# Kernel tuning notes

Measured on AMD Instinct MI355X. Metric: run time of the kernel, lower is better.

Reference implementation:

```python
import jax, jax.numpy as jnp
from jax import lax
import numpy as np


def _conv1d(x, w, b):
    # x: (N, C, L), w: (O, I, K), stride 2, padding 1 -> matches nn.Conv1d(k=4, s=2, p=1)
    y = lax.conv_general_dilated(x, w, window_strides=(2,), padding=[(1, 1)],
                                 dimension_numbers=('NCH', 'OIH', 'NCH'))
    return y + b[None, :, None]


def setup_inputs() -> dict:
    key = jax.random.key(0)
    k = jax.random.split(key, 6)
    B, C_in, T = 32, 256, 2048
    H, D, K_codes = 1024, 512, 1024
    s = 0.02
    return {
        'x': jax.random.normal(k[0], (B, C_in, T), dtype=jnp.float32),
        'w1': jax.random.normal(k[1], (H, C_in, 4), dtype=jnp.float32) * s,
        'b1': jnp.zeros((H,), dtype=jnp.float32),
        'w2': jax.random.normal(k[2], (D, H, 4), dtype=jnp.float32) * s,
        'b2': jnp.zeros((D,), dtype=jnp.float32),
        'codebook': jax.random.normal(k[3], (K_codes, D), dtype=jnp.float32) * s,
    }


def reference(x, w1, b1, w2, b2, codebook):
    z_e = _conv1d(jax.nn.relu(_conv1d(x, w1, b1)), w2, b2)  # (B, D, T/4)
    B, D, T = z_e.shape
    flat = z_e.transpose(0, 2, 1).reshape(-1, D)  # (B*T, D)
    # squared Euclidean distance; argmin identical to cdist(p=2) argmin
    d2 = (jnp.sum(flat * flat, axis=1, keepdims=True)
          - 2.0 * flat @ codebook.T
          + jnp.sum(codebook * codebook, axis=1)[None, :])  # (B*T, K)
    encoding_indices = jnp.argmin(d2, axis=1)  # (B*T,)
    # NOTE: faithful to the original .view(z_e.shape) (a raw reshape, no permute back)
    z_q = codebook[encoding_indices].reshape(B, D, T)
    return (z_q, encoding_indices, z_e)
```

## Files before the change

kernel.cpp:

```cpp
#include <hip/hip_runtime.h>
#include <hip/hip_bf16.h>

using f16x8 = __attribute__((ext_vector_type(8))) _Float16;
using f32x4 = __attribute__((ext_vector_type(4))) float;

union PackU { unsigned u; _Float16 h[2]; };

__device__ inline unsigned split_pack(float v) {
    _Float16 h0 = (_Float16)v;
    float r = (v - (float)h0) * 4096.0f;
    PackU p; p.h[0] = h0; p.h[1] = (_Float16)r;
    return p.u;
}

__device__ __forceinline__ void gll16(const uint4* g, uint4* l) {
    __builtin_amdgcn_global_load_lds(
        (const __attribute__((address_space(1))) uint4*)g,
        (__attribute__((address_space(3))) uint4*)l, 16, 0, 0);
}

__global__ __launch_bounds__(256) void split_kernel(const float* __restrict__ src,
                                                    unsigned* __restrict__ dst, int n4) {
    int g = blockIdx.x * 256 + threadIdx.x;
    if (g >= n4) return;
    float4 v = reinterpret_cast<const float4*>(src)[g];
    uint4 o;
    o.x = split_pack(v.x); o.y = split_pack(v.y);
    o.z = split_pack(v.z); o.w = split_pack(v.w);
    reinterpret_cast<uint4*>(dst)[g] = o;
}

__global__ __launch_bounds__(256) void bsplit_gll(const float* __restrict__ src,
        uint4* __restrict__ dst, int KK, int nTilesK, int total) {
    int tid = blockIdx.x * 256 + threadIdx.x;
    if (tid >= total) return;
    int w = tid & 1023;
    int tile = tid >> 10;
    int kstep = tile % nTilesK;
    int npanel = tile / nTilesK;
    int r = w >> 3, c = w & 7;
    int cp = c ^ (r & 7);
    int p = cp >> 2, kg = cp & 3;
    int n = npanel * 128 + r;
    int k = kstep * 32 + kg * 8;
    const float* s = src + (size_t)n * KK + k;
    uint4 o;
    ushort* h = (ushort*)&o;
#pragma unroll
    for (int j = 0; j < 8; j++) {
        unsigned u = split_pack(s[j]);
        h[j] = p ? (ushort)(u >> 16) : (ushort)u;
    }
    dst[tid] = o;
}

#define BMt 128
#define BNt 128
#define BKt 32

__global__ __launch_bounds__(256, 2) void mfma_gemm(
    const unsigned* __restrict__ Ap, const uint4* __restrict__ Bg,
    const float* __restrict__ bias,
    unsigned* __restrict__ OutP, float* __restrict__ OutF,
    int M, int N, int KK, int nTilesK, int Cc, int L, int Lout, int LoutSh,
    int gatherMode, int mode)
{
    __shared__ uint4 As4[2][BMt * 8];
    __shared__ uint4 Bs4[2][BNt * 8];

    const int tid = threadIdx.x;
    const int m0 = blockIdx.y * BMt;
    const int n0 = blockIdx.x * BNt;

    const int srow = tid >> 1;
    const int kh = tid & 1;
    const int sw_s = srow & 7;
    const int am = m0 + srow;
    const int ab = am >> LoutSh;
    const int at = am & (Lout - 1);
    const unsigned* aprow = Ap + (size_t)ab * Cc * L;
    const int ai0 = 2 * at - 1;
    const unsigned* adir = Ap + (size_t)am * KK;

    const int lane = tid & 63;
    const int wv = tid >> 6;
    const int wr = wv >> 1, wc = wv & 1;
    const int l15 = lane & 15, lq = lane >> 4;

    const uint4* bsrc = Bg + (size_t)blockIdx.x * nTilesK * 1024;

    f32x4 acc0[4][4] = {{{0.f}}};
    f32x4 acc1[4][4] = {{{0.f}}};

    uint4 pa[4];

    auto loadT = [&](int k0) {
        if (gatherMode) {
            int cbase = (k0 >> 2) + kh * 4;
#pragma unroll
            for (int cl = 0; cl < 4; cl++) {
                const unsigned* base = aprow + (size_t)(cbase + cl) * L;
                unsigned q0 = 0, q3 = 0;
                if (ai0 >= 0) q0 = base[ai0];
                unsigned q1 = base[ai0 + 1];
                unsigned q2 = base[ai0 + 2];
                if (ai0 + 3 < L) q3 = base[ai0 + 3];
                pa[cl].x = q0; pa[cl].y = q1; pa[cl].z = q2; pa[cl].w = q3;
            }
        } else {
            const uint4* s = reinterpret_cast<const uint4*>(adir + k0 + kh * 16);
#pragma unroll
            for (int q = 0; q < 4; q++) pa[q] = s[q];
        }
    };

    auto stage = [&](int buf) {
#pragma unroll
        for (int ch = 0; ch < 2; ch++) {
            uint4 w0, w1;
            unsigned* W0 = (unsigned*)&w0; unsigned* W1 = (unsigned*)&w1;
#pragma unroll
            for (int j = 0; j < 4; j++) {
                int e0 = ch * 8 + 2 * j, e1 = e0 + 1;
                unsigned lo = ((const unsigned*)&pa[e0 >> 2])[e0 & 3];
                unsigned hi = ((const unsigned*)&pa[e1 >> 2])[e1 & 3];
                W0[j] = __builtin_amdgcn_perm(hi, lo, 0x05040100u);
                W1[j] = __builtin_amdgcn_perm(hi, lo, 0x07060302u);
            }
            int kc = kh * 2 + ch;
            As4[buf][srow * 8 + ((kc) ^ sw_s)] = w0;
            As4[buf][srow * 8 + ((4 + kc) ^ sw_s)] = w1;
        }
    };

    auto gllB = [&](int buf, int kt2) {
        const uint4* ts = bsrc + (size_t)kt2 * 1024 + wv * 256 + lane;
#pragma unroll
        for (int i = 0; i < 4; i++)
            gll16(ts + i * 64, &Bs4[buf][wv * 256 + i * 64]);
    };

    const int NT = KK / BKt;

    loadT(0);
    gllB(0, 0);
    stage(0);

    for (int kt = 0; kt < NT; kt++) {
        const int cur = kt & 1;
        if (kt + 1 < NT) loadT((kt + 1) * BKt);

        if (kt + 1 < NT) {
            if (gatherMode) asm volatile("s_waitcnt vmcnt(16)" ::: "memory");
            else            asm volatile("s_waitcnt vmcnt(4)" ::: "memory");
        } else {
            asm volatile("s_waitcnt vmcnt(0)" ::: "memory");
        }
        asm volatile("s_waitcnt lgkmcnt(0)\n\ts_barrier" ::: "memory");
        __builtin_amdgcn_sched_barrier(0);

        if (kt + 1 < NT) gllB(cur ^ 1, kt + 1);

        f16x8 a0f[4], a1f[4];
#pragma unroll
        for (int mf = 0; mf < 4; mf++) {
            int row = wr * 64 + mf * 16 + l15;
            int sw = row & 7;
            a0f[mf] = *reinterpret_cast<const f16x8*>(&As4[cur][row * 8 + (lq ^ sw)]);
            a1f[mf] = *reinterpret_cast<const f16x8*>(&As4[cur][row * 8 + ((4 + lq) ^ sw)]);
        }
        __builtin_amdgcn_s_setprio(1);
#pragma unroll
        for (int nf = 0; nf < 4; nf++) {
            int row = wc * 64 + nf * 16 + l15;
            int sw = row & 7;
            f16x8 b0f = *reinterpret_cast<const f16x8*>(&Bs4[cur][row * 8 + (lq ^ sw)]);
            f16x8 b1f = *reinterpret_cast<const f16x8*>(&Bs4[cur][row * 8 + ((4 + lq) ^ sw)]);
#pragma unroll
            for (int mf = 0; mf < 4; mf++) {
                acc0[mf][nf] = __builtin_amdgcn_mfma_f32_16x16x32_f16(
                    a0f[mf], b0f, acc0[mf][nf], 0, 0, 0);
                acc1[mf][nf] = __builtin_amdgcn_mfma_f32_16x16x32_f16(
                    a0f[mf], b1f, acc1[mf][nf], 0, 0, 0);
                acc1[mf][nf] = __builtin_amdgcn_mfma_f32_16x16x32_f16(
                    a1f[mf], b0f, acc1[mf][nf], 0, 0, 0);
            }
        }
        __builtin_amdgcn_s_setprio(0);

        if (kt + 1 < NT) stage(cur ^ 1);
    }

    const float s12 = 1.0f / 4096.0f;
    const int LoutM = Lout - 1;

    if (mode == 2) {
#pragma unroll
        for (int mf = 0; mf < 4; mf++) {
            int mb = m0 + wr * 64 + mf * 16 + lq * 4;
#pragma unroll
            for (int nf = 0; nf < 4; nf++) {
                int n = n0 + wc * 64 + nf * 16 + l15;
#pragma unroll
                for (int r = 0; r < 4; r++) {
                    float v = acc0[mf][nf][r] + acc1[mf][nf][r] * s12;
                    OutF[(size_t)(mb + r) * N + n] = v;
                }
            }
        }
    } else if (mode == 0) {
#pragma unroll
        for (int mf = 0; mf < 4; mf++) {
            int mb = m0 + wr * 64 + mf * 16 + lq * 4;
            int b = mb >> LoutSh, t = mb & LoutM;
#pragma unroll
            for (int nf = 0; nf < 4; nf++) {
                int n = n0 + wc * 64 + nf * 16 + l15;
                float bv = bias[n];
                uint4 o;
                unsigned* O = (unsigned*)&o;
#pragma unroll
                for (int r = 0; r < 4; r++) {
                    float v = acc0[mf][nf][r] + acc1[mf][nf][r] * s12 + bv;
                    v = fmaxf(v, 0.f);
                    O[r] = split_pack(v);
                }
                *reinterpret_cast<uint4*>(&OutP[((size_t)b * N + n) * Lout + t]) = o;
            }
        }
    } else {
#pragma unroll
        for (int mf = 0; mf < 4; mf++) {
            int mb = m0 + wr * 64 + mf * 16 + lq * 4;
            int b = mb >> LoutSh, t = mb & LoutM;
#pragma unroll
            for (int nf = 0; nf < 4; nf++) {
                int n = n0 + wc * 64 + nf * 16 + l15;
                float bv = bias[n];
                float4 f;
                unsigned O[4];
#pragma unroll
                for (int r = 0; r < 4; r++) {
                    float v = acc0[mf][nf][r] + acc1[mf][nf][r] * s12 + bv;
                    ((float*)&f)[r] = v;
                    O[r] = split_pack(v);
                }
                *reinterpret_cast<float4*>(&OutF[((size_t)b * N + n) * Lout + t]) = f;
#pragma unroll
                for (int r = 0; r < 4; r++)
                    OutP[(size_t)(mb + r) * N + n] = O[r];
            }
        }
    }
}

__global__ __launch_bounds__(64) void cb_norm(const float* __restrict__ cb,
                                              float* __restrict__ cn2) {
    int n = blockIdx.x;
    int lane = threadIdx.x;
    float s = 0.f;
    for (int d = lane; d < 512; d += 64) {
        float v = cb[(size_t)n * 512 + d];
        s += v * v;
    }
#pragma unroll
    for (int off = 32; off; off >>= 1) s += __shfl_down(s, off);
    if (lane == 0) cn2[n] = s;
}

__global__ __launch_bounds__(256) void argmin_k(const float* __restrict__ S,
                                                const float* __restrict__ cn2,
                                                float* __restrict__ idxf,
                                                int* __restrict__ idxi, int rows) {
    int wid = threadIdx.x >> 6;
    int lane = threadIdx.x & 63;
    int r = blockIdx.x * 4 + wid;
    if (r >= rows) return;
    const float* srow = S + (size_t)r * 1024;
    float best = INFINITY;
    int bi = 0;
#pragma unroll
    for (int it = 0; it < 4; it++) {
        int nb = it * 256 + lane * 4;
        float4 s4 = *reinterpret_cast<const float4*>(&srow[nb]);
        float4 c4 = *reinterpret_cast<const float4*>(&cn2[nb]);
        float v;
        v = c4.x - 2.f * s4.x; if (v < best) { best = v; bi = nb + 0; }
        v = c4.y - 2.f * s4.y; if (v < best) { best = v; bi = nb + 1; }
        v = c4.z - 2.f * s4.z; if (v < best) { best = v; bi = nb + 2; }
        v = c4.w - 2.f * s4.w; if (v < best) { best = v; bi = nb + 3; }
    }
#pragma unroll
    for (int off = 32; off; off >>= 1) {
        float ov = __shfl_down(best, off);
        int oi = __shfl_down(bi, off);
        if (ov < best || (ov == best && oi < bi)) { best = ov; bi = oi; }
    }
    if (lane == 0) {
        idxf[r] = (float)bi;
        idxi[r] = bi;
    }
}

__global__ __launch_bounds__(256) void gather_k(const int* __restrict__ idx,
                                                const float* __restrict__ cb,
                                                float* __restrict__ zq, int total4) {
    int g = blockIdx.x * 256 + threadIdx.x;
    if (g >= total4) return;
    int r = g >> 7;
    int d4 = g & 127;
    int id = idx[r];
    *reinterpret_cast<float4*>(&zq[(size_t)r * 512 + (size_t)d4 * 4]) =
        *reinterpret_cast<const float4*>(&cb[(size_t)id * 512 + (size_t)d4 * 4]);
}

extern "C" void kernel_launch(void* const* d_in, const int* in_sizes, int n_in,
                              void* d_out, int out_size, void* d_ws, size_t ws_size,
                              hipStream_t stream) {
    const float* x  = (const float*)d_in[0];
    const float* w1 = (const float*)d_in[1];
    const float* b1 = (const float*)d_in[2];
    const float* w2 = (const float*)d_in[3];
    const float* b2 = (const float*)d_in[4];
    const float* cb = (const float*)d_in[5];
    float* out = (float*)d_out;

    const int B = 32, Cin = 256, T = 2048, H = 1024, D = 512, Kc = 1024;
    const int T1 = 1024, T2 = 512;

    float* zq_out  = out;
    float* idx_out = out + (size_t)B * T2 * D;
    float* ze_out  = idx_out + (size_t)B * T2;

    unsigned* w1f = (unsigned*)d_ws;
    unsigned* w2f = w1f + (size_t)H * Cin * 4;
    unsigned* cbf = w2f + (size_t)D * H * 4;
    float* cn2    = (float*)(cbf + (size_t)Kc * D);
    int* idx_ws   = (int*)(cn2 + Kc);
    unsigned* dyn = (unsigned*)(idx_ws + B * T2);

    size_t fixed_u32 = (size_t)H * Cin * 4 + (size_t)D * H * 4 + (size_t)Kc * D
                       + Kc + (size_t)B * T2 + 256;
    int NB = 32;
    while (NB > 1 &&
           (fixed_u32 + (size_t)NB * ((size_t)Cin * T + (size_t)H * T1 + (size_t)T2 * D))
               * 4 > ws_size)
        NB >>= 1;

    unsigned* xp = dyn;
    unsigned* hp = xp + (size_t)NB * Cin * T;
    unsigned* zp = hp + (size_t)NB * H * T1;
    float* S = (float*)hp;

    bsplit_gll<<<(H * (Cin * 4) / 4 + 255) / 256, 256, 0, stream>>>(
        w1, (uint4*)w1f, Cin * 4, (Cin * 4) / 32, H * (Cin * 4) / 4);
    bsplit_gll<<<(D * (H * 4) / 4 + 255) / 256, 256, 0, stream>>>(
        w2, (uint4*)w2f, H * 4, (H * 4) / 32, D * (H * 4) / 4);
    bsplit_gll<<<(Kc * D / 4 + 255) / 256, 256, 0, stream>>>(
        cb, (uint4*)cbf, D, D / 32, Kc * D / 4);
    cb_norm<<<Kc, 64, 0, stream>>>(cb, cn2);

    for (int b0 = 0; b0 < B; b0 += NB) {
        int nb = (B - b0 < NB) ? (B - b0) : NB;

        split_kernel<<<(nb * Cin * T / 4 + 255) / 256, 256, 0, stream>>>(
            x + (size_t)b0 * Cin * T, xp, nb * Cin * T / 4);

        mfma_gemm<<<dim3(H / BNt, nb * T1 / BMt), 256, 0, stream>>>(
            xp, (const uint4*)w1f, b1, hp, nullptr,
            nb * T1, H, Cin * 4, (Cin * 4) / 32, Cin, T, T1, 10, 1, 0);

        mfma_gemm<<<dim3(D / BNt, nb * T2 / BMt), 256, 0, stream>>>(
            hp, (const uint4*)w2f, b2, zp, ze_out + (size_t)b0 * D * T2,
            nb * T2, D, H * 4, (H * 4) / 32, H, T1, T2, 9, 1, 1);

        mfma_gemm<<<dim3(Kc / BNt, nb * T2 / BMt), 256, 0, stream>>>(
            zp, (const uint4*)cbf, nullptr, nullptr, S,
            nb * T2, Kc, D, D / 32, D, T2, T2, 9, 0, 2);

        argmin_k<<<(nb * T2 + 3) / 4, 256, 0, stream>>>(
            S, cn2, idx_out + (size_t)b0 * T2, idx_ws, nb * T2);

        gather_k<<<(nb * T2 * D / 4 + 255) / 256, 256, 0, stream>>>(
            idx_ws, cb, zq_out + (size_t)b0 * T2 * D, nb * T2 * D / 4);
    }
}
```

Before: 579.2 us.

## Reschedule GEMM main loop to interleave staging between two MFMA phases

The K-loop now issues both the next A-tile register load and the B global-to-LDS copy at the top of each iteration. The MFMA work is split into an acc0 phase and an acc1 phase, with the LDS staging of the next A tile placed between them so the global loads have time to land. The wait and barrier move to the end of the iteration, using a full vmcnt(0) wait instead of the previous partial waits. This is meant to overlap memory traffic with matrix math better. The trade-off is that the full drain at the end of each iteration may expose load latency, and holding extra fragments in registers may raise register pressure.

```diff
diff --git a/kernel.cpp b/kernel.cpp
--- a/kernel.cpp
+++ b/kernel.cpp
@@ -145,50 +145,72 @@
     loadT(0);
     gllB(0, 0);
     stage(0);
+    asm volatile("s_waitcnt vmcnt(0)" ::: "memory");
+    asm volatile("s_waitcnt lgkmcnt(0)\n\ts_barrier" ::: "memory");
+    __builtin_amdgcn_sched_barrier(0);
 
     for (int kt = 0; kt < NT; kt++) {
         const int cur = kt & 1;
-        if (kt + 1 < NT) loadT((kt + 1) * BKt);
-
-        if (kt + 1 < NT) {
-            if (gatherMode) asm volatile("s_waitcnt vmcnt(16)" ::: "memory");
-            else            asm volatile("s_waitcnt vmcnt(4)" ::: "memory");
-        } else {
-            asm volatile("s_waitcnt vmcnt(0)" ::: "memory");
-        }
-        asm volatile("s_waitcnt lgkmcnt(0)\n\ts_barrier" ::: "memory");
-        __builtin_amdgcn_sched_barrier(0);
-
-        if (kt + 1 < NT) gllB(cur ^ 1, kt + 1);
-
-        f16x8 a0f[4], a1f[4];
+        const bool more = (kt + 1 < NT);
+        if (more) {
+            loadT((kt + 1) * BKt);
+            gllB(cur ^ 1, kt + 1);
+        }
+
+        f16x8 a0f[4], b0f[4];
 #pragma unroll
         for (int mf = 0; mf < 4; mf++) {
             int row = wr * 64 + mf * 16 + l15;
-            int sw = row & 7;
-            a0f[mf] = *reinterpret_cast<const f16x8*>(&As4[cur][row * 8 + (lq ^ sw)]);
-            a1f[mf] = *reinterpret_cast<const f16x8*>(&As4[cur][row * 8 + ((4 + lq) ^ sw)]);
-        }
-        __builtin_amdgcn_s_setprio(1);
+            a0f[mf] = *reinterpret_cast<const f16x8*>(
+                &As4[cur][row * 8 + (lq ^ (row & 7))]);
+        }
 #pragma unroll
         for (int nf = 0; nf < 4; nf++) {
             int row = wc * 64 + nf * 16 + l15;
-            int sw = row & 7;
-            f16x8 b0f = *reinterpret_cast<const f16x8*>(&Bs4[cur][row * 8 + (lq ^ sw)]);
-            f16x8 b1f = *reinterpret_cast<const f16x8*>(&Bs4[cur][row * 8 + ((4 + lq) ^ sw)]);
-#pragma unroll
-            for (int mf = 0; mf < 4; mf++) {
+            b0f[nf] = *reinterpret_cast<const f16x8*>(
+                &Bs4[cur][row * 8 + (lq ^ (row & 7))]);
+        }
+        __builtin_amdgcn_s_setprio(1);
+#pragma unroll
+        for (int nf = 0; nf < 4; nf++)
+#pragma unroll
+            for (int mf = 0; mf < 4; mf++)
                 acc0[mf][nf] = __builtin_amdgcn_mfma_f32_16x16x32_f16(
-                    a0f[mf], b0f, acc0[mf][nf], 0, 0, 0);
+                    a0f[mf], b0f[nf], acc0[mf][nf], 0, 0, 0);
+        __builtin_amdgcn_s_setprio(0);
+
+        __builtin_amdgcn_sched_barrier(0);
+        if (more) stage(cur ^ 1);
+        __builtin_amdgcn_sched_barrier(0);
+
+        __builtin_amdgcn_s_setprio(1);
+#pragma unroll
+        for (int nf = 0; nf < 4; nf++) {
+            int row = wc * 64 + nf * 16 + l15;
+            f16x8 b1f = *reinterpret_cast<const f16x8*>(
+                &Bs4[cur][row * 8 + ((4 + lq) ^ (row & 7))]);
+#pragma unroll
+            for (int mf = 0; mf < 4; mf++)
                 acc1[mf][nf] = __builtin_amdgcn_mfma_f32_16x16x32_f16(
                     a0f[mf], b1f, acc1[mf][nf], 0, 0, 0);
+        }
+#pragma unroll
+        for (int mf = 0; mf < 4; mf++) {
+            int row = wr * 64 + mf * 16 + l15;
+            f16x8 a1f = *reinterpret_cast<const f16x8*>(
+                &As4[cur][row * 8 + ((4 + lq) ^ (row & 7))]);
+#pragma unroll
+            for (int nf = 0; nf < 4; nf++)
                 acc1[mf][nf] = __builtin_amdgcn_mfma_f32_16x16x32_f16(
-                    a1f[mf], b0f, acc1[mf][nf], 0, 0, 0);
-            }
+                    a1f, b0f[nf], acc1[mf][nf], 0, 0, 0);
         }
         __builtin_amdgcn_s_setprio(0);
 
-        if (kt + 1 < NT) stage(cur ^ 1);
+        if (more) {
+            asm volatile("s_waitcnt vmcnt(0)" ::: "memory");
+            asm volatile("s_waitcnt lgkmcnt(0)\n\ts_barrier" ::: "memory");
+            __builtin_amdgcn_sched_barrier(0);
+        }
     }
 
     const float s12 = 1.0f / 4096.0f;
```

New measurement: 613.8 us. 1.06x slower.

## Fuse input split into conv GEMM and argmin into distance GEMM epilogue

Applied to the files above, without the earlier changes.

Drops the separate fp32-to-split-fp16 pass over x: the first conv GEMM now reads raw fp32 input and splits it while staging into LDS. The distance GEMM no longer writes the full score matrix. Its epilogue computes cn2 - 2s, packs the value and index into a sortable 64-bit key, reduces across lanes and does an atomicMin per row. The argmin and gather kernels are merged into one finalize kernel. This removes large intermediate reads and writes and kernel launches, at the cost of extra conversion ALU work in staging, 64-bit atomics, and a memset.

```diff
diff --git a/kernel.cpp b/kernel.cpp
--- a/kernel.cpp
+++ b/kernel.cpp
@@ -17,17 +17,6 @@
     __builtin_amdgcn_global_load_lds(
         (const __attribute__((address_space(1))) uint4*)g,
         (__attribute__((address_space(3))) uint4*)l, 16, 0, 0);
-}
-
-__global__ __launch_bounds__(256) void split_kernel(const float* __restrict__ src,
-                                                    unsigned* __restrict__ dst, int n4) {
-    int g = blockIdx.x * 256 + threadIdx.x;
-    if (g >= n4) return;
-    float4 v = reinterpret_cast<const float4*>(src)[g];
-    uint4 o;
-    o.x = split_pack(v.x); o.y = split_pack(v.y);
-    o.z = split_pack(v.z); o.w = split_pack(v.w);
-    reinterpret_cast<uint4*>(dst)[g] = o;
 }
 
 __global__ __launch_bounds__(256) void bsplit_gll(const float* __restrict__ src,
@@ -62,8 +51,9 @@
     const unsigned* __restrict__ Ap, const uint4* __restrict__ Bg,
     const float* __restrict__ bias,
     unsigned* __restrict__ OutP, float* __restrict__ OutF,
+    const float* __restrict__ cn2v, unsigned long long* __restrict__ mk,
     int M, int N, int KK, int nTilesK, int Cc, int L, int Lout, int LoutSh,
-    int gatherMode, int mode)
+    int gatherMode, int aFp32, int mode)
 {
     __shared__ uint4 As4[2][BMt * 8];
     __shared__ uint4 Bs4[2][BNt * 8];
@@ -115,6 +105,19 @@
     };
 
     auto stage = [&](int buf) {
+        uint4 pp[4];
+#pragma unroll
+        for (int q = 0; q < 4; q++) {
+            if (aFp32) {
+                const unsigned* s = (const unsigned*)&pa[q];
+                unsigned* d = (unsigned*)&pp[q];
+#pragma unroll
+                for (int j = 0; j < 4; j++)
+                    d[j] = split_pack(__uint_as_float(s[j]));
+            } else {
+                pp[q] = pa[q];
+            }
+        }
 #pragma unroll
         for (int ch = 0; ch < 2; ch++) {
             uint4 w0, w1;
@@ -122,8 +125,8 @@
 #pragma unroll
             for (int j = 0; j < 4; j++) {
                 int e0 = ch * 8 + 2 * j, e1 = e0 + 1;
-                unsigned lo = ((const unsigned*)&pa[e0 >> 2])[e0 & 3];
-                unsigned hi = ((const unsigned*)&pa[e1 >> 2])[e1 & 3];
+                unsigned lo = ((const unsigned*)&pp[e0 >> 2])[e0 & 3];
+                unsigned hi = ((const unsigned*)&pp[e1 >> 2])[e1 & 3];
                 W0[j] = __builtin_amdgcn_perm(hi, lo, 0x05040100u);
                 W1[j] = __builtin_amdgcn_perm(hi, lo, 0x07060302u);
             }
@@ -197,15 +200,26 @@
     if (mode == 2) {
 #pragma unroll
         for (int mf = 0; mf < 4; mf++) {
-            int mb = m0 + wr * 64 + mf * 16 + lq * 4;
-#pragma unroll
-            for (int nf = 0; nf < 4; nf++) {
-                int n = n0 + wc * 64 + nf * 16 + l15;
-#pragma unroll
-                for (int r = 0; r < 4; r++) {
-                    float v = acc0[mf][nf][r] + acc1[mf][nf][r] * s12;
-                    OutF[(size_t)(mb + r) * N + n] = v;
+#pragma unroll
+            for (int r = 0; r < 4; r++) {
+                int row = m0 + wr * 64 + mf * 16 + lq * 4 + r;
+                unsigned long long best = ~0ull;
+#pragma unroll
+                for (int nf = 0; nf < 4; nf++) {
+                    int n = n0 + wc * 64 + nf * 16 + l15;
+                    float s = acc0[mf][nf][r] + acc1[mf][nf][r] * s12;
+                    float v = cn2v[n] - 2.f * s;
+                    unsigned u = __float_as_uint(v);
+                    unsigned sk = (u & 0x80000000u) ? ~u : (u | 0x80000000u);
+                    unsigned long long key = ((unsigned long long)sk << 32) | (unsigned)n;
+                    if (key < best) best = key;
                 }
+#pragma unroll
+                for (int msk = 1; msk < 16; msk <<= 1) {
+                    unsigned long long o = __shfl_xor(best, msk);
+                    if (o < best) best = o;
+                }
+                if (l15 == 0) atomicMin(&mk[row], best);
             }
         }
     } else if (mode == 0) {
@@ -268,48 +282,15 @@
     if (lane == 0) cn2[n] = s;
 }
 
-__global__ __launch_bounds__(256) void argmin_k(const float* __restrict__ S,
-                                                const float* __restrict__ cn2,
-                                                float* __restrict__ idxf,
-                                                int* __restrict__ idxi, int rows) {
-    int wid = threadIdx.x >> 6;
-    int lane = threadIdx.x & 63;
-    int r = blockIdx.x * 4 + wid;
-    if (r >= rows) return;
-    const float* srow = S + (size_t)r * 1024;
-    float best = INFINITY;
-    int bi = 0;
-#pragma unroll
-    for (int it = 0; it < 4; it++) {
-        int nb = it * 256 + lane * 4;
-        float4 s4 = *reinterpret_cast<const float4*>(&srow[nb]);
-        float4 c4 = *reinterpret_cast<const float4*>(&cn2[nb]);
-        float v;
-        v = c4.x - 2.f * s4.x; if (v < best) { best = v; bi = nb + 0; }
-        v = c4.y - 2.f * s4.y; if (v < best) { best = v; bi = nb + 1; }
-        v = c4.z - 2.f * s4.z; if (v < best) { best = v; bi = nb + 2; }
-        v = c4.w - 2.f * s4.w; if (v < best) { best = v; bi = nb + 3; }
-    }
-#pragma unroll
-    for (int off = 32; off; off >>= 1) {
-        float ov = __shfl_down(best, off);
-        int oi = __shfl_down(bi, off);
-        if (ov < best || (ov == best && oi < bi)) { best = ov; bi = oi; }
-    }
-    if (lane == 0) {
-        idxf[r] = (float)bi;
-        idxi[r] = bi;
-    }
-}
-
-__global__ __launch_bounds__(256) void gather_k(const int* __restrict__ idx,
-                                                const float* __restrict__ cb,
-                                                float* __restrict__ zq, int total4) {
+__global__ __launch_bounds__(256) void finalize_k(
+        const unsigned long long* __restrict__ mk, const float* __restrict__ cb,
+        float* __restrict__ idxf, float* __restrict__ zq, int total4) {
     int g = blockIdx.x * 256 + threadIdx.x;
     if (g >= total4) return;
     int r = g >> 7;
     int d4 = g & 127;
-    int id = idx[r];
+    int id = (int)(unsigned)(mk[r] & 0xffffffffu);
+    if (d4 == 0) idxf[r] = (float)id;
     *reinterpret_cast<float4*>(&zq[(size_t)r * 512 + (size_t)d4 * 4]) =
         *reinterpret_cast<const float4*>(&cb[(size_t)id * 512 + (size_t)d4 * 4]);
 }
@@ -336,21 +317,19 @@
     unsigned* w2f = w1f + (size_t)H * Cin * 4;
     unsigned* cbf = w2f + (size_t)D * H * 4;
     float* cn2    = (float*)(cbf + (size_t)Kc * D);
-    int* idx_ws   = (int*)(cn2 + Kc);
-    unsigned* dyn = (unsigned*)(idx_ws + B * T2);
+    unsigned long long* mk = (unsigned long long*)(cn2 + Kc + 2);
+    unsigned* dyn = (unsigned*)(mk + (size_t)B * T2);
 
     size_t fixed_u32 = (size_t)H * Cin * 4 + (size_t)D * H * 4 + (size_t)Kc * D
-                       + Kc + (size_t)B * T2 + 256;
+                       + Kc + 2 * (size_t)B * T2 + 256;
     int NB = 32;
     while (NB > 1 &&
-           (fixed_u32 + (size_t)NB * ((size_t)Cin * T + (size_t)H * T1 + (size_t)T2 * D))
+           (fixed_u32 + (size_t)NB * ((size_t)H * T1 + (size_t)T2 * D))
                * 4 > ws_size)
         NB >>= 1;
 
-    unsigned* xp = dyn;
-    unsigned* hp = xp + (size_t)NB * Cin * T;
+    unsigned* hp = dyn;
     unsigned* zp = hp + (size_t)NB * H * T1;
-    float* S = (float*)hp;
 
     bsplit_gll<<<(H * (Cin * 4) / 4 + 255) / 256, 256, 0, stream>>>(
         w1, (uint4*)w1f, Cin * 4, (Cin * 4) / 32, H * (Cin * 4) / 4);
@@ -359,29 +338,28 @@
     bsplit_gll<<<(Kc * D / 4 + 255) / 256, 256, 0, stream>>>(
         cb, (uint4*)cbf, D, D / 32, Kc * D / 4);
     cb_norm<<<Kc, 64, 0, stream>>>(cb, cn2);
+    hipMemsetAsync(mk, 0xFF, (size_t)B * T2 * 8, stream);
 
     for (int b0 = 0; b0 < B; b0 += NB) {
         int nb = (B - b0 < NB) ? (B - b0) : NB;
 
-        split_kernel<<<(nb * Cin * T / 4 + 255) / 256, 256, 0, stream>>>(
-            x + (size_t)b0 * Cin * T, xp, nb * Cin * T / 4);
-
         mfma_gemm<<<dim3(H / BNt, nb * T1 / BMt), 256, 0, stream>>>(
-            xp, (const uint4*)w1f, b1, hp, nullptr,
-            nb * T1, H, Cin * 4, (Cin * 4) / 32, Cin, T, T1, 10, 1, 0);
+            (const unsigned*)(x + (size_t)b0 * Cin * T), (const uint4*)w1f, b1,
+            hp, nullptr, nullptr, nullptr,
+            nb * T1, H, Cin * 4, (Cin * 4) / 32, Cin, T, T1, 10, 1, 1, 0);
 
         mfma_gemm<<<dim3(D / BNt, nb * T2 / BMt), 256, 0, stream>>>(
             hp, (const uint4*)w2f, b2, zp, ze_out + (size_t)b0 * D * T2,
-            nb * T2, D, H * 4, (H * 4) / 32, H, T1, T2, 9, 1, 1);
+            nullptr, nullptr,
+            nb * T2, D, H * 4, (H * 4) / 32, H, T1, T2, 9, 1, 0, 1);
 
         mfma_gemm<<<dim3(Kc / BNt, nb * T2 / BMt), 256, 0, stream>>>(
-            zp, (const uint4*)cbf, nullptr, nullptr, S,
-            nb * T2, Kc, D, D / 32, D, T2, T2, 9, 0, 2);
-
-        argmin_k<<<(nb * T2 + 3) / 4, 256, 0, stream>>>(
-            S, cn2, idx_out + (size_t)b0 * T2, idx_ws, nb * T2);
-
-        gather_k<<<(nb * T2 * D / 4 + 255) / 256, 256, 0, stream>>>(
-            idx_ws, cb, zq_out + (size_t)b0 * T2 * D, nb * T2 * D / 4);
-    }
-}
+            zp, (const uint4*)cbf, nullptr, nullptr, nullptr,
+            cn2, mk + (size_t)b0 * T2,
+            nb * T2, Kc, D, D / 32, D, T2, T2, 9, 0, 0, 2);
+
+        finalize_k<<<(nb * T2 * D / 4 + 255) / 256, 256, 0, stream>>>(
+            mk + (size_t)b0 * T2, cb, idx_out + (size_t)b0 * T2,
+            zq_out + (size_t)b0 * T2 * D, nb * T2 * D / 4);
+    }
+}
```

After: 720.8 us. +24.5%, slower.
